# Kernel tuning notes

Measured on AMD Instinct MI355X. Metric: run time of the kernel, lower is better.

The kernel has to match this reference:

```python
import jax, jax.numpy as jnp
import numpy as np

B, D, R = 256, 4096, 8
MAX_R = 2 * R - 1  # static upper bound on radius (torch uses data-dependent max)


def setup_inputs() -> dict:
    key = jax.random.key(0)
    ks = jax.random.split(key, 6)
    x = jax.random.randint(ks[0], (B, D), 0, 2).astype(jnp.float32)  # binary spins
    W = jax.random.normal(ks[1], (D, D), jnp.float32) / np.float32(np.sqrt(D))
    b = jax.random.normal(ks[2], (D,), jnp.float32)
    radius_raw = jax.random.randint(ks[3], (B, 1), 0, MAX_R)  # +1 in reference -> [1, 2R-1]
    gumbel_u = jax.random.uniform(ks[4], (B, D), jnp.float32)
    u = jax.random.uniform(ks[5], (B,), jnp.float32)
    return {"x": x, "W": W, "b": b, "radius_raw": radius_raw, "gumbel_u": gumbel_u, "u": u}


def _model(x, W, b):
    # quadratic pseudo-Boolean energy model: per-sample scalar score
    return 0.5 * jnp.einsum('bi,ij,bj->b', x, W, x) + x @ b


def reference(x, W, b, radius_raw, gumbel_u, u):
    radius = radius_raw + 1                                   # [B,1] in [1, 2R-1]
    r_mask = (jnp.arange(MAX_R)[None, :] < radius).astype(x.dtype)  # [B, MAX_R]

    score_x = _model(x, W, b)                                 # [B]
    grad = jax.lax.stop_gradient(
        jax.grad(lambda xx: _model(xx, W, b).sum())(x))       # [B,D], detached

    delta_x = -(2.0 * x - 1.0)
    score_change_x = delta_x * grad / 2.0                     # logits of proposal

    # multinomial without replacement == Gumbel top-k on the logits
    eps = 1e-10
    g = -jnp.log(-jnp.log(jnp.clip(gumbel_u, eps, 1.0 - eps)))
    _, indices = jax.lax.top_k(score_change_x + g, MAX_R)     # [B, MAX_R]

    rows = jnp.arange(B)[:, None]
    cur_bits = x[rows, indices]                               # gather
    new_bits = 1.0 - cur_bits
    y = x.at[rows, indices].set(r_mask * new_bits + (1.0 - r_mask) * cur_bits)

    delta_y = -(2.0 * y - 1.0)
    score_y = _model(y, W, b)
    score_change_y = delta_y * grad / 2.0

    log_pypx = score_y - score_x
    log_tilde_pxpy = -jnp.sum(grad * (y - x), axis=-1)
    log_zxzy = (jax.scipy.special.logsumexp(score_change_x, axis=-1)
                - jax.scipy.special.logsumexp(score_change_y, axis=-1))
    log_acc = jnp.minimum(log_pypx + log_tilde_pxpy + log_zxzy, 0.0)

    accepted = (jnp.exp(log_acc) > u).astype(x.dtype)[:, None]  # [B,1]
    return y * accepted + (1.0 - accepted) * x
```

## Files before the change

### kernel.cpp

```cpp
#include <hip/hip_runtime.h>

#define Bsz 256
#define Dd  4096
#define MAXR 15
#define FMAX 3.402823466e+38f
#define BK 64
#define LSTRIDE 72

typedef short bf16x8 __attribute__((ext_vector_type(8)));
typedef float f32x4  __attribute__((ext_vector_type(4)));

__device__ __forceinline__ unsigned short f2bf(float f) {
    unsigned int u = __float_as_uint(f);
    unsigned int r = (u + 0x7fffu + ((u >> 16) & 1u)) >> 16;
    return (unsigned short)r;
}
__device__ __forceinline__ float bf2f(unsigned short h) {
    return __uint_as_float(((unsigned int)h) << 16);
}

__global__ __launch_bounds__(256) void k_ssym(const float* __restrict__ W,
                                              const float* __restrict__ x,
                                              unsigned short* __restrict__ shi,
                                              unsigned short* __restrict__ slo,
                                              unsigned short* __restrict__ xb) {
    __shared__ float t1[64][68];
    __shared__ float t2[64][68];
    int bid = blockIdx.x;
    int bi = 0;
    while (bid >= 64 - bi) { bid -= 64 - bi; ++bi; }
    const int bj = bi + bid;
    const int i0 = bi * 64, j0 = bj * 64;
    const int tid = threadIdx.x;

    #pragma unroll
    for (int sb = 0; sb < 4; ++sb) {
        int s = sb * 256 + tid;
        int r = s >> 4, q = (s & 15) * 4;
        *(float4*)&t1[r][q] = *(const float4*)(W + (size_t)(i0 + r) * Dd + j0 + q);
        *(float4*)&t2[r][q] = *(const float4*)(W + (size_t)(j0 + r) * Dd + i0 + q);
    }
    __syncthreads();

    const int r = tid >> 2, c0 = (tid & 3) * 16;
    {
        unsigned short vh[16], vl[16];
        #pragma unroll
        for (int k = 0; k < 16; ++k) {
            float s = 0.5f * (t1[r][c0 + k] + t2[c0 + k][r]);
            vh[k] = f2bf(s);
            vl[k] = f2bf(s - bf2f(vh[k]));
        }
        size_t o = (size_t)(i0 + r) * Dd + j0 + c0;
        *(uint4*)(shi + o) = *(const uint4*)&vh[0];
        *(uint4*)(shi + o + 8) = *(const uint4*)&vh[8];
        *(uint4*)(slo + o) = *(const uint4*)&vl[0];
        *(uint4*)(slo + o + 8) = *(const uint4*)&vl[8];
    }
    if (bi != bj) {
        unsigned short vh[16], vl[16];
        #pragma unroll
        for (int k = 0; k < 16; ++k) {
            float s = 0.5f * (t2[r][c0 + k] + t1[c0 + k][r]);
            vh[k] = f2bf(s);
            vl[k] = f2bf(s - bf2f(vh[k]));
        }
        size_t o = (size_t)(j0 + r) * Dd + i0 + c0;
        *(uint4*)(shi + o) = *(const uint4*)&vh[0];
        *(uint4*)(shi + o + 8) = *(const uint4*)&vh[8];
        *(uint4*)(slo + o) = *(const uint4*)&vl[0];
        *(uint4*)(slo + o + 8) = *(const uint4*)&vl[8];
    }

    if (blockIdx.x < 256) {
        const float* xp = x + (size_t)blockIdx.x * 4096;
        unsigned short* xo = xb + (size_t)blockIdx.x * 4096;
        #pragma unroll
        for (int c = 0; c < 4; ++c) {
            int e = c * 1024 + tid * 4;
            float4 v = *(const float4*)(xp + e);
            unsigned short o4[4] = { f2bf(v.x), f2bf(v.y), f2bf(v.z), f2bf(v.w) };
            *(uint2*)(xo + e) = *(const uint2*)o4;
        }
    }
}

__global__ __launch_bounds__(128) void k_gemm(const unsigned short* __restrict__ xb,
                                              const unsigned short* __restrict__ shi,
                                              const unsigned short* __restrict__ slo,
                                              float* __restrict__ part,
                                              int kchunk) {
    __shared__ __align__(16) unsigned short As[64 * LSTRIDE];
    __shared__ __align__(16) unsigned short Bh[64 * LSTRIDE];
    __shared__ __align__(16) unsigned short Bl[64 * LSTRIDE];
    const int tid = threadIdx.x;
    const int n0 = blockIdx.x * 64, m0 = blockIdx.y * 64;
    const int kbase = blockIdx.z * kchunk;
    const int w = tid >> 6, lane = tid & 63;
    const int ln = lane & 15, quad = lane >> 4;

    unsigned ga[4], gb[4];
    int lofs[4];
    #pragma unroll
    for (int j = 0; j < 4; ++j) {
        int s = tid + j * 128;
        int r = s >> 3, g = s & 7;
        ga[j]   = (unsigned)((m0 + r) * Dd + kbase + g * 8);
        gb[j]   = (unsigned)((n0 + r) * Dd + kbase + g * 8);
        lofs[j] = r * LSTRIDE + g * 8;
    }

    f32x4 acc[4][2];
    #pragma unroll
    for (int mt = 0; mt < 4; ++mt)
        #pragma unroll
        for (int ct = 0; ct < 2; ++ct)
            #pragma unroll
            for (int rr = 0; rr < 4; ++rr) acc[mt][ct][rr] = 0.0f;

    bf16x8 va[4], vh[4], vl[4];
    #pragma unroll
    for (int j = 0; j < 4; ++j) {
        va[j] = *(const bf16x8*)(xb  + ga[j]);
        vh[j] = *(const bf16x8*)(shi + gb[j]);
        vl[j] = *(const bf16x8*)(slo + gb[j]);
    }

    for (int k0 = 0; k0 < kchunk; k0 += BK) {
        __syncthreads();
        #pragma unroll
        for (int j = 0; j < 4; ++j) {
            *(bf16x8*)&As[lofs[j]] = va[j];
            *(bf16x8*)&Bh[lofs[j]] = vh[j];
            *(bf16x8*)&Bl[lofs[j]] = vl[j];
        }
        {
            int kn = k0 + BK;
            int ks = (kn < kchunk) ? kn : 0;
            #pragma unroll
            for (int j = 0; j < 4; ++j) {
                va[j] = *(const bf16x8*)(xb  + ga[j] + ks);
                vh[j] = *(const bf16x8*)(shi + gb[j] + ks);
                vl[j] = *(const bf16x8*)(slo + gb[j] + ks);
            }
        }
        __syncthreads();
        #pragma unroll
        for (int kk = 0; kk < BK; kk += 32) {
            const int gr = (kk >> 3) + quad;
            bf16x8 a[4];
            #pragma unroll
            for (int mt = 0; mt < 4; ++mt)
                a[mt] = *(const bf16x8*)&As[(mt * 16 + ln) * LSTRIDE + gr * 8];
            #pragma unroll
            for (int ct = 0; ct < 2; ++ct) {
                int rb = w * 32 + ct * 16 + ln;
                bf16x8 bh = *(const bf16x8*)&Bh[rb * LSTRIDE + gr * 8];
                bf16x8 bl = *(const bf16x8*)&Bl[rb * LSTRIDE + gr * 8];
                #pragma unroll
                for (int mt = 0; mt < 4; ++mt) {
                    acc[mt][ct] = __builtin_amdgcn_mfma_f32_16x16x32_bf16(a[mt], bh, acc[mt][ct], 0, 0, 0);
                    acc[mt][ct] = __builtin_amdgcn_mfma_f32_16x16x32_bf16(a[mt], bl, acc[mt][ct], 0, 0, 0);
                }
            }
        }
    }
    float* prow = part + (size_t)blockIdx.z * (Bsz * Dd);
    #pragma unroll
    for (int mt = 0; mt < 4; ++mt)
        #pragma unroll
        for (int ct = 0; ct < 2; ++ct)
            #pragma unroll
            for (int rr = 0; rr < 4; ++rr) {
                int m = m0 + mt * 16 + quad * 4 + rr;
                int n = n0 + w * 32 + ct * 16 + ln;
                prow[(size_t)m * Dd + n] = acc[mt][ct][rr];
            }
}

__device__ __forceinline__ float block_max256(float v, float* redf) {
    #pragma unroll
    for (int off = 32; off; off >>= 1) v = fmaxf(v, __shfl_down(v, off));
    __syncthreads();
    if ((threadIdx.x & 63) == 0) redf[threadIdx.x >> 6] = v;
    __syncthreads();
    return fmaxf(fmaxf(redf[0], redf[1]), fmaxf(redf[2], redf[3]));
}
__device__ __forceinline__ float block_sum256(float v, float* redf) {
    #pragma unroll
    for (int off = 32; off; off >>= 1) v += __shfl_down(v, off);
    __syncthreads();
    if ((threadIdx.x & 63) == 0) redf[threadIdx.x >> 6] = v;
    __syncthreads();
    return (redf[0] + redf[1]) + (redf[2] + redf[3]);
}

__global__ __launch_bounds__(256, 1) void k_epilogue(const float* __restrict__ x,
                                                  const float* __restrict__ W,
                                                  const int* __restrict__ radius_raw,
                                                  const float* __restrict__ gu,
                                                  const float* __restrict__ uvec,
                                                  const float* __restrict__ part,
                                                  const float* __restrict__ bias,
                                                  float* __restrict__ out,
                                                  int nsplit) {
    __shared__ float scx_s[Dd];
    __shared__ float redf[2][4];
    __shared__ int   redi[2][4];
    __shared__ float redsum[4];
    __shared__ int   flips[MAXR];

    const int b = blockIdx.x;
    const int tid = threadIdx.x;
    const float* xrow  = x  + (size_t)b * Dd;
    const float* gurow = gu + (size_t)b * Dd;

    float4 g4[4], bs4[4], xv4[4], uu4[4];
    #pragma unroll
    for (int c = 0; c < 4; ++c) {
        int j = c * 1024 + tid * 4;
        g4[c]  = *(const float4*)(part + (size_t)b * Dd + j);
        bs4[c] = *(const float4*)(bias + j);
        xv4[c] = *(const float4*)(xrow + j);
        uu4[c] = *(const float4*)(gurow + j);
    }
    if (nsplit == 4) {
        float4 p1[4], p2[4], p3[4];
        #pragma unroll
        for (int c = 0; c < 4; ++c) {
            int j = c * 1024 + tid * 4;
            p1[c] = *(const float4*)(part + (size_t)(1 * Bsz + b) * Dd + j);
            p2[c] = *(const float4*)(part + (size_t)(2 * Bsz + b) * Dd + j);
            p3[c] = *(const float4*)(part + (size_t)(3 * Bsz + b) * Dd + j);
        }
        #pragma unroll
        for (int c = 0; c < 4; ++c) {
            g4[c].x = ((g4[c].x + p1[c].x) + p2[c].x) + p3[c].x;
            g4[c].y = ((g4[c].y + p1[c].y) + p2[c].y) + p3[c].y;
            g4[c].z = ((g4[c].z + p1[c].z) + p2[c].z) + p3[c].z;
            g4[c].w = ((g4[c].w + p1[c].w) + p2[c].w) + p3[c].w;
        }
    } else {
        for (int z = 1; z < nsplit; ++z) {
            const float* pz = part + (size_t)z * (Bsz * Dd) + (size_t)b * Dd;
            #pragma unroll
            for (int c = 0; c < 4; ++c) {
                float4 a = *(const float4*)(pz + c * 1024 + tid * 4);
                g4[c].x += a.x; g4[c].y += a.y; g4[c].z += a.z; g4[c].w += a.w;
            }
        }
    }
    float sc[16], ky[16];
    float lmax = -FMAX;
    float lkey = -FMAX; int lidx = 0x7fffffff;
    #pragma unroll
    for (int c = 0; c < 4; ++c) {
        const float* gg = (const float*)&g4[c];
        const float* gc = (const float*)&bs4[c];
        const float* gx = (const float*)&xv4[c];
        const float* gup = (const float*)&uu4[c];
        #pragma unroll
        for (int e = 0; e < 4; ++e) {
            int r = c * 4 + e;
            float g = gg[e] + gc[e];
            float s = (1.0f - 2.0f * gx[e]) * g * 0.5f;
            float k = s - logf(-logf(fmaxf(gup[e], 1e-10f)));
            sc[r] = s;
            ky[r] = k;
            lmax = fmaxf(lmax, s);
            if (k > lkey) { lkey = k; lidx = c * 1024 + tid * 4 + e; }
        }
        *(float4*)&scx_s[c * 1024 + tid * 4] = *(const float4*)&sc[c * 4];
    }

    float mx = block_max256(lmax, redsum);
    float ls = 0.0f;
    #pragma unroll
    for (int r = 0; r < 16; ++r) ls += expf(sc[r] - mx);
    float sum_x = block_sum256(ls, redsum);
    float lse_x = mx + logf(sum_x);

    const int radius = radius_raw[b] + 1;
    unsigned removed = 0;
    for (int t = 0; t < radius; ++t) {
        float v = lkey; int idx = lidx;
        #pragma unroll
        for (int off = 32; off; off >>= 1) {
            float v2 = __shfl_down(v, off);
            int   i2 = __shfl_down(idx, off);
            if (v2 > v || (v2 == v && i2 < idx)) { v = v2; idx = i2; }
        }
        const int buf = t & 1;
        if ((tid & 63) == 0) { redf[buf][tid >> 6] = v; redi[buf][tid >> 6] = idx; }
        __syncthreads();
        float bv = redf[buf][0]; int bi = redi[buf][0];
        #pragma unroll
        for (int w2 = 1; w2 < 4; ++w2) {
            float v2 = redf[buf][w2]; int i2 = redi[buf][w2];
            if (v2 > bv || (v2 == bv && i2 < bi)) { bv = v2; bi = i2; }
        }
        if (tid == ((bi >> 2) & 255)) {
            removed |= 1u << (((bi >> 10) << 2) | (bi & 3));
            lkey = -FMAX; lidx = 0x7fffffff;
            #pragma unroll
            for (int c = 0; c < 4; ++c)
                #pragma unroll
                for (int e = 0; e < 4; ++e) {
                    int r = c * 4 + e;
                    if (!(removed & (1u << r)) && ky[r] > lkey) {
                        lkey = ky[r]; lidx = c * 1024 + tid * 4 + e;
                    }
                }
        }
        if (tid == 0) flips[t] = bi;
    }
    __syncthreads();

    float delta = 0.0f;
    if (tid < radius) {
        float sv = scx_s[flips[tid]];
        delta = expf(-sv - mx) - expf(sv - mx);
    }
    float sum_y = sum_x + block_sum256(delta, redsum);
    float lse_y = mx + logf(sum_y);

    float ts = 0.0f;
    for (int t = tid; t < radius * radius; t += 256) {
        int p = flips[t / radius], q = flips[t % radius];
        float dp = 1.0f - 2.0f * xrow[p];
        float dq = 1.0f - 2.0f * xrow[q];
        ts += 0.25f * dp * dq * (W[(size_t)p * Dd + q] + W[(size_t)q * Dd + p]);
    }
    float T = block_sum256(ts, redsum);

    float log_acc = fminf(T + lse_x - lse_y, 0.0f);
    int accepted = (expf(log_acc) > uvec[b]) ? 1 : 0;

    float* orow = out + (size_t)b * Dd;
    #pragma unroll
    for (int c = 0; c < 4; ++c)
        *(float4*)(orow + c * 1024 + tid * 4) = xv4[c];
    __syncthreads();
    if (accepted && tid < radius) {
        int p = flips[tid];
        orow[p] = 1.0f - xrow[p];
    }
}

extern "C" void kernel_launch(void* const* d_in, const int* in_sizes, int n_in,
                              void* d_out, int out_size, void* d_ws, size_t ws_size,
                              hipStream_t stream) {
    const float* x          = (const float*)d_in[0];
    const float* W          = (const float*)d_in[1];
    const float* bias       = (const float*)d_in[2];
    const int*   radius_raw = (const int*)d_in[3];
    const float* gu         = (const float*)d_in[4];
    const float* u          = (const float*)d_in[5];
    float* out = (float*)d_out;

    unsigned short* shi = (unsigned short*)d_ws;
    unsigned short* slo = shi + (size_t)Dd * Dd;
    unsigned short* xb  = slo + (size_t)Dd * Dd;
    float*          prt = (float*)(xb + (size_t)Bsz * Dd);

    const size_t fixed = (size_t)2 * Dd * Dd * 2 + (size_t)Bsz * Dd * 2;
    const int nsplit = (ws_size >= fixed + (size_t)4 * Bsz * Dd * 4) ? 4 : 2;
    const int kchunk = Dd / nsplit;

    k_ssym<<<2080, 256, 0, stream>>>(W, x, shi, slo, xb);
    k_gemm<<<dim3(64, 4, nsplit), 128, 0, stream>>>(xb, shi, slo, prt, kchunk);
    k_epilogue<<<Bsz, 256, 0, stream>>>(x, W, radius_raw, gu, u, prt, bias, out, nsplit);
}
```

Measured before the change: 173.5 us.

## Enlarge GEMM tile to cover full batch per block, sharing B tiles

Each GEMM block now covers all 256 batch rows against a 64-column slice of the split W, using 512 threads (8 waves arranged 4x2) instead of 128 threads on a 64x64 tile. The hi/lo W tiles are loaded once per block and reused across the whole batch instead of being re-read by four separate M blocks, which cuts global and L2 traffic for the dominant operand. The trade-off is a 4x smaller grid (64 x nsplit blocks), which may leave compute units idle, plus more LDS per block.

Measured after the change: 168.5 us. 2.9% less time.

```diff
diff --git a/kernel.cpp b/kernel.cpp
--- a/kernel.cpp
+++ b/kernel.cpp
@@ -85,30 +85,32 @@
     }
 }
 
-__global__ __launch_bounds__(128) void k_gemm(const unsigned short* __restrict__ xb,
+__global__ __launch_bounds__(512, 2) void k_gemm(const unsigned short* __restrict__ xb,
                                               const unsigned short* __restrict__ shi,
                                               const unsigned short* __restrict__ slo,
                                               float* __restrict__ part,
                                               int kchunk) {
-    __shared__ __align__(16) unsigned short As[64 * LSTRIDE];
+    __shared__ __align__(16) unsigned short As[256 * LSTRIDE];
     __shared__ __align__(16) unsigned short Bh[64 * LSTRIDE];
     __shared__ __align__(16) unsigned short Bl[64 * LSTRIDE];
     const int tid = threadIdx.x;
-    const int n0 = blockIdx.x * 64, m0 = blockIdx.y * 64;
+    const int n0 = blockIdx.x * 64;
     const int kbase = blockIdx.z * kchunk;
     const int w = tid >> 6, lane = tid & 63;
     const int ln = lane & 15, quad = lane >> 4;
-
-    unsigned ga[4], gb[4];
-    int lofs[4];
+    const int wm = w >> 1, wn = w & 1;
+
+    unsigned ga[4]; int la[4];
     #pragma unroll
     for (int j = 0; j < 4; ++j) {
-        int s = tid + j * 128;
+        int s = tid + j * 512;
         int r = s >> 3, g = s & 7;
-        ga[j]   = (unsigned)((m0 + r) * Dd + kbase + g * 8);
-        gb[j]   = (unsigned)((n0 + r) * Dd + kbase + g * 8);
-        lofs[j] = r * LSTRIDE + g * 8;
-    }
+        ga[j] = (unsigned)(r * Dd + kbase + g * 8);
+        la[j] = r * LSTRIDE + g * 8;
+    }
+    const int rb2 = tid >> 3, gb2 = tid & 7;
+    const unsigned gb = (unsigned)((n0 + rb2) * Dd + kbase + gb2 * 8);
+    const int lb = rb2 * LSTRIDE + gb2 * 8;
 
     f32x4 acc[4][2];
     #pragma unroll
@@ -118,31 +120,25 @@
             #pragma unroll
             for (int rr = 0; rr < 4; ++rr) acc[mt][ct][rr] = 0.0f;
 
-    bf16x8 va[4], vh[4], vl[4];
-    #pragma unroll
-    for (int j = 0; j < 4; ++j) {
-        va[j] = *(const bf16x8*)(xb  + ga[j]);
-        vh[j] = *(const bf16x8*)(shi + gb[j]);
-        vl[j] = *(const bf16x8*)(slo + gb[j]);
-    }
+    bf16x8 va[4], vh, vl;
+    #pragma unroll
+    for (int j = 0; j < 4; ++j) va[j] = *(const bf16x8*)(xb + ga[j]);
+    vh = *(const bf16x8*)(shi + gb);
+    vl = *(const bf16x8*)(slo + gb);
 
     for (int k0 = 0; k0 < kchunk; k0 += BK) {
         __syncthreads();
         #pragma unroll
-        for (int j = 0; j < 4; ++j) {
-            *(bf16x8*)&As[lofs[j]] = va[j];
-            *(bf16x8*)&Bh[lofs[j]] = vh[j];
-            *(bf16x8*)&Bl[lofs[j]] = vl[j];
-        }
+        for (int j = 0; j < 4; ++j) *(bf16x8*)&As[la[j]] = va[j];
+        *(bf16x8*)&Bh[lb] = vh;
+        *(bf16x8*)&Bl[lb] = vl;
         {
             int kn = k0 + BK;
             int ks = (kn < kchunk) ? kn : 0;
             #pragma unroll
-            for (int j = 0; j < 4; ++j) {
-                va[j] = *(const bf16x8*)(xb  + ga[j] + ks);
-                vh[j] = *(const bf16x8*)(shi + gb[j] + ks);
-                vl[j] = *(const bf16x8*)(slo + gb[j] + ks);
-            }
+            for (int j = 0; j < 4; ++j) va[j] = *(const bf16x8*)(xb + ga[j] + ks);
+            vh = *(const bf16x8*)(shi + gb + ks);
+            vl = *(const bf16x8*)(slo + gb + ks);
         }
         __syncthreads();
         #pragma unroll
@@ -151,10 +147,10 @@
             bf16x8 a[4];
             #pragma unroll
             for (int mt = 0; mt < 4; ++mt)
-                a[mt] = *(const bf16x8*)&As[(mt * 16 + ln) * LSTRIDE + gr * 8];
+                a[mt] = *(const bf16x8*)&As[(wm * 64 + mt * 16 + ln) * LSTRIDE + gr * 8];
             #pragma unroll
             for (int ct = 0; ct < 2; ++ct) {
-                int rb = w * 32 + ct * 16 + ln;
+                int rb = wn * 32 + ct * 16 + ln;
                 bf16x8 bh = *(const bf16x8*)&Bh[rb * LSTRIDE + gr * 8];
                 bf16x8 bl = *(const bf16x8*)&Bl[rb * LSTRIDE + gr * 8];
                 #pragma unroll
@@ -172,8 +168,8 @@
         for (int ct = 0; ct < 2; ++ct)
             #pragma unroll
             for (int rr = 0; rr < 4; ++rr) {
-                int m = m0 + mt * 16 + quad * 4 + rr;
-                int n = n0 + w * 32 + ct * 16 + ln;
+                int m = wm * 64 + mt * 16 + quad * 4 + rr;
+                int n = n0 + wn * 32 + ct * 16 + ln;
                 prow[(size_t)m * Dd + n] = acc[mt][ct][rr];
             }
 }
@@ -368,6 +364,6 @@
     const int kchunk = Dd / nsplit;
 
     k_ssym<<<2080, 256, 0, stream>>>(W, x, shi, slo, xb);
-    k_gemm<<<dim3(64, 4, nsplit), 128, 0, stream>>>(xb, shi, slo, prt, kchunk);
+    k_gemm<<<dim3(64, 1, nsplit), 512, 0, stream>>>(xb, shi, slo, prt, kchunk);
     k_epilogue<<<Bsz, 256, 0, stream>>>(x, W, radius_raw, gu, u, prt, bias, out, nsplit);
 }
```
